# Performance work log

Hardware: AMD Instinct MI355X
Metric: run time of the kernel (lower is better)

## Reference

```python
import jax, jax.numpy as jnp
import numpy as np


def setup_inputs() -> dict:
    key = jax.random.key(0)
    ks = jax.random.split(key, 8)
    B, N = 4, 256
    E, C, H = 64, 128, 256
    return {
        "edge_features": jax.random.normal(ks[0], (B, E, N, N), dtype=jnp.float32),
        "node_features": jax.random.normal(ks[1], (B, C, N), dtype=jnp.float32),
        "W1": jax.random.normal(ks[2], (H, E + 2 * C), dtype=jnp.float32) * 0.05,
        "b1": jax.random.normal(ks[3], (H,), dtype=jnp.float32) * 0.05,
        "W2": jax.random.normal(ks[4], (H, H), dtype=jnp.float32) * 0.05,
        "b2": jax.random.normal(ks[5], (H,), dtype=jnp.float32) * 0.05,
        "W3": jax.random.normal(ks[6], (1, H), dtype=jnp.float32) * 0.05,
        "b3": jax.random.normal(ks[7], (1,), dtype=jnp.float32) * 0.05,
    }


def reference(edge_features, node_features, W1, b1, W2, b2, W3, b3):
    B, C, N = node_features.shape
    # node_addon_row: [B, C, N, N] broadcast along last dim; col along dim 2
    row = jnp.broadcast_to(node_features[:, :, :, None], (B, C, N, N))
    col = jnp.broadcast_to(node_features[:, :, None, :], (B, C, N, N))
    x = jnp.concatenate([edge_features, row, col], axis=1)  # [B, E+2C, N, N]
    # 1x1 conv == channel matmul
    x = jax.nn.relu(jnp.einsum('bcnm,oc->bonm', x, W1) + b1[None, :, None, None])
    x = jax.nn.relu(jnp.einsum('bcnm,oc->bonm', x, W2) + b2[None, :, None, None])
    x = jnp.einsum('bcnm,oc->bonm', x, W3) + b3[None, :, None, None]  # [B,1,N,N]
    return x[:, 0, :, :]
```

## Files before the change

kernel.cpp:

```cpp
#include <hip/hip_runtime.h>
#include <stdint.h>

typedef __bf16 bf16x8 __attribute__((ext_vector_type(8)));
typedef __bf16 bf16x4v __attribute__((ext_vector_type(4)));
typedef float  f32x16 __attribute__((ext_vector_type(16)));
typedef float  f32x4t __attribute__((ext_vector_type(4)));
typedef unsigned int u32x2 __attribute__((ext_vector_type(2)));

#define WS_W1S 0
#define WS_W2S 32768
#define WS_R   163840
#define WS_CT  1212416

__global__ __launch_bounds__(256) void prep_all(
    const float* __restrict__ W1, const float* __restrict__ b1,
    const float* __restrict__ W2, const float* __restrict__ node,
    __bf16* __restrict__ w1s, __bf16* __restrict__ w2s,
    float* __restrict__ Rt, __bf16* __restrict__ Ctb) {
    __shared__ float nds[128 * 4];
    const int blk = blockIdx.x;
    if (blk < 40) {
        int t = blk * 256 + threadIdx.x;
        int chunk = t >> 6, lane = t & 63;
        if (chunk < 128) {
            int wid = chunk >> 5, ks = (chunk >> 1) & 15, mb = chunk & 1;
            int o = wid * 64 + mb * 32 + (lane & 31);
            int k = ks * 16 + (lane >> 5) * 8;
            const float* src = W2 + o * 256 + k;
            __bf16* dst = w2s + chunk * 512 + lane * 8;
#pragma unroll
            for (int j = 0; j < 8; ++j) dst[j] = (__bf16)src[j];
        } else if (chunk < 160) {
            int c1 = chunk - 128;
            int wid = c1 >> 3, ks = (c1 >> 1) & 3, mb = c1 & 1;
            int o = wid * 64 + mb * 32 + (lane & 31);
            int k = ks * 16 + (lane >> 5) * 8;
            const float* src = W1 + o * 320 + k;
            __bf16* dst = w1s + c1 * 512 + lane * 8;
#pragma unroll
            for (int j = 0; j < 8; ++j) dst[j] = (__bf16)src[j];
        }
        return;
    }
    const int rcb = blk - 40;
    const int b = rcb >> 6, j0 = (rcb & 63) << 2;
    const int o = threadIdx.x;
    if (o < 128)
        *(float4*)&nds[o * 4] = *(const float4*)(node + b * 32768 + o * 256 + j0);
    __syncthreads();
    float aR[4] = {0.f, 0.f, 0.f, 0.f};
    float aC[4] = {0.f, 0.f, 0.f, 0.f};
    const float* wr = W1 + o * 320 + 64;
    const float* wc = W1 + o * 320 + 192;
    for (int c4 = 0; c4 < 32; ++c4) {
        float4 wrv = *(const float4*)(wr + c4 * 4);
        float4 wcv = *(const float4*)(wc + c4 * 4);
        const float* wrp = (const float*)&wrv;
        const float* wcp = (const float*)&wcv;
#pragma unroll
        for (int r = 0; r < 4; ++r) {
            f32x4t n4 = *(const f32x4t*)&nds[(c4 * 4 + r) * 4];
#pragma unroll
            for (int q = 0; q < 4; ++q) {
                aR[q] = fmaf(wrp[r], n4[q], aR[q]);
                aC[q] = fmaf(wcp[r], n4[q], aC[q]);
            }
        }
    }
    float bb = b1[o];
#pragma unroll
    for (int j = 0; j < 4; ++j) {
        int idx = ((b * 256 + j0 + j) << 8) + o;
        Rt[idx] = aR[j] + bb;
        Ctb[idx] = (__bf16)aC[j];
    }
}

__device__ __forceinline__ void lds_barrier() {
    __builtin_amdgcn_sched_barrier(0);
    asm volatile("s_waitcnt lgkmcnt(0)" ::: "memory");
    __builtin_amdgcn_s_barrier();
    __builtin_amdgcn_sched_barrier(0);
}

__global__ __launch_bounds__(256, 2) void fused_main(
    const float* __restrict__ edge, const __bf16* __restrict__ w1s,
    const __bf16* __restrict__ w2s, const float* __restrict__ Rt,
    const __bf16* __restrict__ Ctb, const float* __restrict__ b2,
    const float* __restrict__ W3, const float* __restrict__ b3,
    float* __restrict__ out) {
    __shared__ unsigned int lds_e[64 * 34];
    __shared__ unsigned int lds_h1[64 * 140];
    __shared__ float lds_p[8 * 64 * 9];
    __shared__ float lds_c[512];

    const int tid = threadIdx.x;
    const int wid = tid >> 6;
    const int lane = tid & 63;
    const int p31 = lane & 31;
    const int hi = lane >> 5;
    const int obase = wid * 64;

    const int blk = blockIdx.x;
    const int b   = blk >> 7;
    const int m0  = ((blk >> 5) & 3) << 6;
    const int n0  = (blk & 31) << 3;

    lds_c[tid] = b2[tid];
    lds_c[256 + tid] = W3[tid];

    const float4* eg = (const float4*)edge;
    const int a_ = tid & 15;
    const int epb = tid >> 4;
    float4 pf[4];

#define PREFETCH(nn)                                                        \
    {                                                                       \
        _Pragma("unroll")                                                   \
        for (int r = 0; r < 2; ++r) {                                       \
            int ep = r * 16 + epb;                                          \
            int f4 = (b * 64 + ep * 2) * 16384 + (nn) * 64 + (m0 >> 2) + a_;\
            pf[r * 2]     = eg[f4];                                         \
            pf[r * 2 + 1] = eg[f4 + 16384];                                 \
        }                                                                   \
    }

#define LOAD_Q(bf, q)                                                       \
    {                                                                       \
        _Pragma("unroll")                                                   \
        for (int ksl = 0; ksl < 4; ++ksl)                                   \
            _Pragma("unroll")                                               \
            for (int mb = 0; mb < 2; ++mb)                                  \
                A2q[bf][ksl][mb] = *(const bf16x8*)(w2_s +                  \
                    ((((wid << 4) + (q) * 4 + ksl) << 1) + mb) * 512 + (lane << 3)); \
    }

    PREFETCH(n0);

    bf16x4v CvR[8][2];
#pragma unroll
    for (int mb = 0; mb < 2; ++mb)
#pragma unroll
        for (int rg = 0; rg < 4; ++rg)
#pragma unroll
            for (int nb = 0; nb < 2; ++nb)
                CvR[mb * 4 + rg][nb] = *(const bf16x4v*)(Ctb +
                    ((b * 256 + m0 + nb * 32 + p31) << 8) + obase + mb * 32 + 8 * rg + 4 * hi);

    bf16x8 A1[2][4];
#pragma unroll
    for (int mb = 0; mb < 2; ++mb)
#pragma unroll
        for (int ks = 0; ks < 4; ++ks)
            A1[mb][ks] = *(const bf16x8*)(w1s +
                ((((wid << 2) + ks) << 1) + mb) * 512 + (lane << 3));

    f32x16 acc[2][2];
    bf16x8 A2q[2][4][2];
    for (int it = 0; it < 8; ++it) {
        const int n = n0 + it;

        uint64_t w2a = (uint64_t)w2s;
        asm volatile("" : "+s"(w2a));
        const __bf16* w2_s = (const __bf16*)w2a;

#pragma unroll
        for (int r = 0; r < 2; ++r) {
            int ep = r * 16 + epb;
            const float* p0 = (const float*)&pf[r * 2];
            const float* p1 = (const float*)&pf[r * 2 + 1];
#pragma unroll
            for (int i = 0; i < 4; ++i) {
                union { __bf16 h[2]; unsigned int u; } t;
                t.h[0] = (__bf16)p0[i];
                t.h[1] = (__bf16)p1[i];
                lds_e[(a_ * 4 + i) * 34 + ep] = t.u;
            }
        }
        if (it < 7) PREFETCH(n + 1);

        const int nRow = (b * 256 + n) << 8;
        f32x4t Rv[2][4];
#pragma unroll
        for (int mb = 0; mb < 2; ++mb)
#pragma unroll
            for (int rg = 0; rg < 4; ++rg)
                Rv[mb][rg] = *(const f32x4t*)(Rt + nRow + obase + mb * 32 + 8 * rg + 4 * hi);

#pragma unroll
        for (int mb = 0; mb < 2; ++mb)
#pragma unroll
            for (int nb = 0; nb < 2; ++nb)
#pragma unroll
                for (int rg = 0; rg < 4; ++rg)
#pragma unroll
                    for (int rr = 0; rr < 4; ++rr)
                        acc[mb][nb][rg * 4 + rr] = (float)CvR[mb * 4 + rg][nb][rr];

        lds_barrier();

        __builtin_amdgcn_s_setprio(1);
#pragma unroll
        for (int ks = 0; ks < 4; ++ks) {
            bf16x8 B1[2];
#pragma unroll
            for (int nb = 0; nb < 2; ++nb) {
                union { u32x2 d[2]; bf16x8 v; } bb;
                const unsigned int* base = &lds_e[(nb * 32 + p31) * 34 + ks * 8 + hi * 4];
                bb.d[0] = *(const u32x2*)base;
                bb.d[1] = *(const u32x2*)(base + 2);
                B1[nb] = bb.v;
            }
#pragma unroll
            for (int mb = 0; mb < 2; ++mb) {
                acc[mb][0] = __builtin_amdgcn_mfma_f32_32x32x16_bf16(A1[mb][ks], B1[0], acc[mb][0], 0, 0, 0);
                acc[mb][1] = __builtin_amdgcn_mfma_f32_32x32x16_bf16(A1[mb][ks], B1[1], acc[mb][1], 0, 0, 0);
            }
        }
        __builtin_amdgcn_s_setprio(0);

#pragma unroll
        for (int mb = 0; mb < 2; ++mb) {
#pragma unroll
            for (int rg = 0; rg < 4; ++rg) {
                int och = obase + mb * 32 + 8 * rg + 4 * hi;
                f32x4t Rvv = Rv[mb][rg];
#pragma unroll
                for (int nb = 0; nb < 2; ++nb) {
                    int pix = nb * 32 + p31;
                    union { __bf16 h[4]; u32x2 u; } t;
#pragma unroll
                    for (int rr = 0; rr < 4; ++rr) {
                        float v = acc[mb][nb][rg * 4 + rr] + Rvv[rr];
                        t.h[rr] = (__bf16)fmaxf(v, 0.f);
                    }
                    *(u32x2*)&lds_h1[pix * 140 + (och >> 1)] = t.u;
                }
            }
        }
        LOAD_Q(0, 0);

#pragma unroll
        for (int mb = 0; mb < 2; ++mb)
#pragma unroll
            for (int rg = 0; rg < 4; ++rg) {
                f32x4t b2v = *(const f32x4t*)&lds_c[obase + mb * 32 + 8 * rg + 4 * hi];
#pragma unroll
                for (int nb = 0; nb < 2; ++nb)
#pragma unroll
                    for (int rr = 0; rr < 4; ++rr)
                        acc[mb][nb][rg * 4 + rr] = b2v[rr];
            }

        lds_barrier();

        __builtin_amdgcn_s_setprio(1);
#pragma unroll
        for (int q = 0; q < 4; ++q) {
            if (q < 3) LOAD_Q((q + 1) & 1, q + 1);
#pragma unroll
            for (int ksl = 0; ksl < 4; ++ksl) {
                const int ksg = q * 4 + ksl;
                bf16x8 B2[2];
#pragma unroll
                for (int nb = 0; nb < 2; ++nb)
                    B2[nb] = *(const bf16x8*)&lds_h1[(nb * 32 + p31) * 140 + ksg * 8 + hi * 4];
#pragma unroll
                for (int mb = 0; mb < 2; ++mb) {
                    acc[mb][0] = __builtin_amdgcn_mfma_f32_32x32x16_bf16(A2q[q & 1][ksl][mb], B2[0], acc[mb][0], 0, 0, 0);
                    acc[mb][1] = __builtin_amdgcn_mfma_f32_32x32x16_bf16(A2q[q & 1][ksl][mb], B2[1], acc[mb][1], 0, 0, 0);
                }
            }
        }
        __builtin_amdgcn_s_setprio(0);

        float part0 = 0.f, part1 = 0.f;
#pragma unroll
        for (int mb = 0; mb < 2; ++mb) {
#pragma unroll
            for (int rg = 0; rg < 4; ++rg) {
                int och = obase + mb * 32 + 8 * rg + 4 * hi;
                f32x4t w3v = *(const f32x4t*)&lds_c[256 + och];
#pragma unroll
                for (int rr = 0; rr < 4; ++rr) {
                    float h0 = fmaxf(acc[mb][0][rg * 4 + rr], 0.f);
                    float h1v = fmaxf(acc[mb][1][rg * 4 + rr], 0.f);
                    part0 = fmaf(w3v[rr], h0, part0);
                    part1 = fmaf(w3v[rr], h1v, part1);
                }
            }
        }
        lds_p[(it * 64 + 0 * 32 + p31) * 9 + wid * 2 + hi] = part0;
        lds_p[(it * 64 + 1 * 32 + p31) * 9 + wid * 2 + hi] = part1;
    }

    __syncthreads();
    {
        float bb3 = b3[0];
#pragma unroll
        for (int r = 0; r < 2; ++r) {
            int idx = r * 256 + tid;
            int row = idx >> 6;
            int mm  = idx & 63;
            float s = bb3;
#pragma unroll
            for (int k = 0; k < 8; ++k) s += lds_p[(row * 64 + mm) * 9 + k];
            out[((b * 256 + n0 + row) << 8) + m0 + mm] = s;
        }
    }
#undef PREFETCH
#undef LOAD_Q
}

extern "C" void kernel_launch(void* const* d_in, const int* in_sizes, int n_in,
                              void* d_out, int out_size, void* d_ws, size_t ws_size,
                              hipStream_t stream) {
    const float* edge = (const float*)d_in[0];
    const float* node = (const float*)d_in[1];
    const float* W1   = (const float*)d_in[2];
    const float* b1   = (const float*)d_in[3];
    const float* W2   = (const float*)d_in[4];
    const float* b2   = (const float*)d_in[5];
    const float* W3   = (const float*)d_in[6];
    const float* b3   = (const float*)d_in[7];
    char* ws = (char*)d_ws;
    __bf16* w1s = (__bf16*)(ws + WS_W1S);
    __bf16* w2s = (__bf16*)(ws + WS_W2S);
    float*  Rt  = (float*)(ws + WS_R);
    __bf16* Ctb = (__bf16*)(ws + WS_CT);

    prep_all<<<296, 256, 0, stream>>>(W1, b1, W2, node, w1s, w2s, Rt, Ctb);
    fused_main<<<512, 256, 0, stream>>>(edge, w1s, w2s, Rt, Ctb, b2, W3, b3, (float*)d_out);
}
```

Baseline: 151.5 us.

## Use 512-thread blocks processing two rows, stage half of W2 in LDS, atomically reduce output

Doubles the block to eight waves, with two row-groups sharing one set of W1/W2 fragments, and halves the grid. The upper half of the W2 K-dimension is staged once into LDS and read from there, which cuts register pressure and global reloads of W2. The per-tile cross-wave partial-sum buffer and final reduction are replaced by a shuffle and atomicAdd into the output, which prep_all now pre-initialises with b3. The cost is much larger LDS use per block (about 64KB for W2), which may limit occupancy, plus atomic contention on the output.

```diff
diff --git a/kernel.cpp b/kernel.cpp
--- a/kernel.cpp
+++ b/kernel.cpp
@@ -15,10 +15,17 @@
 __global__ __launch_bounds__(256) void prep_all(
     const float* __restrict__ W1, const float* __restrict__ b1,
     const float* __restrict__ W2, const float* __restrict__ node,
-    __bf16* __restrict__ w1s, __bf16* __restrict__ w2s,
-    float* __restrict__ Rt, __bf16* __restrict__ Ctb) {
+    const float* __restrict__ b3, __bf16* __restrict__ w1s,
+    __bf16* __restrict__ w2s, float* __restrict__ Rt,
+    __bf16* __restrict__ Ctb, float* __restrict__ out) {
     __shared__ float nds[128 * 4];
     const int blk = blockIdx.x;
+    if (blk >= 296) {
+        float v = b3[0];
+        float4 f4 = make_float4(v, v, v, v);
+        *(float4*)(out + (blk - 296) * 1024 + threadIdx.x * 4) = f4;
+        return;
+    }
     if (blk < 40) {
         int t = blk * 256 + threadIdx.x;
         int chunk = t >> 6, lane = t & 63;
@@ -83,35 +90,51 @@
     __builtin_amdgcn_sched_barrier(0);
 }
 
-__global__ __launch_bounds__(256, 2) void fused_main(
+__global__ __launch_bounds__(512, 2) void fused_main(
     const float* __restrict__ edge, const __bf16* __restrict__ w1s,
     const __bf16* __restrict__ w2s, const float* __restrict__ Rt,
     const __bf16* __restrict__ Ctb, const float* __restrict__ b2,
     const float* __restrict__ W3, const float* __restrict__ b3,
     float* __restrict__ out) {
-    __shared__ unsigned int lds_e[64 * 34];
-    __shared__ unsigned int lds_h1[64 * 140];
-    __shared__ float lds_p[8 * 64 * 9];
+    __shared__ __bf16 w2lds[32768];
+    __shared__ unsigned int lds_e[128 * 34];
+    __shared__ unsigned int lds_h1[2][64 * 140];
     __shared__ float lds_c[512];
 
     const int tid = threadIdx.x;
-    const int wid = tid >> 6;
+    const int wid8 = tid >> 6;
+    const int og   = wid8 & 3;
+    const int rw   = wid8 >> 2;
     const int lane = tid & 63;
-    const int p31 = lane & 31;
-    const int hi = lane >> 5;
-    const int obase = wid * 64;
+    const int p31  = lane & 31;
+    const int hi   = lane >> 5;
+    const int obase = og << 6;
 
     const int blk = blockIdx.x;
-    const int b   = blk >> 7;
-    const int m0  = ((blk >> 5) & 3) << 6;
-    const int n0  = (blk & 31) << 3;
-
-    lds_c[tid] = b2[tid];
-    lds_c[256 + tid] = W3[tid];
+    const int b   = blk >> 6;
+    const int m0  = ((blk >> 4) & 3) << 6;
+    const int n0  = (blk & 15) << 4;
+
+    lds_c[tid] = (tid < 256) ? b2[tid] : W3[tid - 256];
+
+    {
+        bf16x8 wt[8];
+#pragma unroll
+        for (int i = 0; i < 8; ++i) {
+            int rc = wid8 * 8 + i;
+            int mb = rc & 1, k8 = (rc >> 1) & 7, wg = rc >> 4;
+            int schunk = (((wg << 4) + 8 + k8) << 1) + mb;
+            wt[i] = *(const bf16x8*)(w2s + schunk * 512 + (lane << 3));
+        }
+#pragma unroll
+        for (int i = 0; i < 8; ++i)
+            *(bf16x8*)(w2lds + (wid8 * 8 + i) * 512 + (lane << 3)) = wt[i];
+    }
 
     const float4* eg = (const float4*)edge;
-    const int a_ = tid & 15;
-    const int epb = tid >> 4;
+    const int tid8 = tid & 255;
+    const int a_   = tid8 & 15;
+    const int epb  = tid8 >> 4;
     float4 pf[4];
 
 #define PREFETCH(nn)                                                        \
@@ -132,10 +155,10 @@
             _Pragma("unroll")                                               \
             for (int mb = 0; mb < 2; ++mb)                                  \
                 A2q[bf][ksl][mb] = *(const bf16x8*)(w2_s +                  \
-                    ((((wid << 4) + (q) * 4 + ksl) << 1) + mb) * 512 + (lane << 3)); \
-    }
-
-    PREFETCH(n0);
+                    ((((og << 4) + (q) * 4 + ksl) << 1) + mb) * 512 + (lane << 3)); \
+    }
+
+    PREFETCH(n0 + rw);
 
     bf16x4v CvR[8][2];
 #pragma unroll
@@ -153,16 +176,19 @@
 #pragma unroll
         for (int ks = 0; ks < 4; ++ks)
             A1[mb][ks] = *(const bf16x8*)(w1s +
-                ((((wid << 2) + ks) << 1) + mb) * 512 + (lane << 3));
+                ((((og << 2) + ks) << 1) + mb) * 512 + (lane << 3));
 
     f32x16 acc[2][2];
     bf16x8 A2q[2][4][2];
-    for (int it = 0; it < 8; ++it) {
-        const int n = n0 + it;
+#pragma unroll 1
+    for (int itp = 0; itp < 8; ++itp) {
+        const int n_r = n0 + itp * 2 + rw;
 
         uint64_t w2a = (uint64_t)w2s;
         asm volatile("" : "+s"(w2a));
         const __bf16* w2_s = (const __bf16*)w2a;
+        int koff = 0;
+        asm volatile("" : "+v"(koff));
 
 #pragma unroll
         for (int r = 0; r < 2; ++r) {
@@ -174,12 +200,12 @@
                 union { __bf16 h[2]; unsigned int u; } t;
                 t.h[0] = (__bf16)p0[i];
                 t.h[1] = (__bf16)p1[i];
-                lds_e[(a_ * 4 + i) * 34 + ep] = t.u;
-            }
-        }
-        if (it < 7) PREFETCH(n + 1);
-
-        const int nRow = (b * 256 + n) << 8;
+                lds_e[(rw * 64 + a_ * 4 + i) * 34 + ep] = t.u;
+            }
+        }
+        if (itp < 7) PREFETCH(n0 + (itp + 1) * 2 + rw);
+
+        const int nRow = (b * 256 + n_r) << 8;
         f32x4t Rv[2][4];
 #pragma unroll
         for (int mb = 0; mb < 2; ++mb)
@@ -206,7 +232,7 @@
 #pragma unroll
             for (int nb = 0; nb < 2; ++nb) {
                 union { u32x2 d[2]; bf16x8 v; } bb;
-                const unsigned int* base = &lds_e[(nb * 32 + p31) * 34 + ks * 8 + hi * 4];
+                const unsigned int* base = &lds_e[(rw * 64 + nb * 32 + p31) * 34 + ks * 8 + hi * 4];
                 bb.d[0] = *(const u32x2*)base;
                 bb.d[1] = *(const u32x2*)(base + 2);
                 B1[nb] = bb.v;
@@ -234,7 +260,7 @@
                         float v = acc[mb][nb][rg * 4 + rr] + Rvv[rr];
                         t.h[rr] = (__bf16)fmaxf(v, 0.f);
                     }
-                    *(u32x2*)&lds_h1[pix * 140 + (och >> 1)] = t.u;
+                    *(u32x2*)&lds_h1[rw][pix * 140 + (och >> 1)] = t.u;
                 }
             }
         }
@@ -256,20 +282,38 @@
 
         __builtin_amdgcn_s_setprio(1);
 #pragma unroll
-        for (int q = 0; q < 4; ++q) {
-            if (q < 3) LOAD_Q((q + 1) & 1, q + 1);
+        for (int q = 0; q < 2; ++q) {
+            if (q == 0) LOAD_Q(1, 1);
 #pragma unroll
             for (int ksl = 0; ksl < 4; ++ksl) {
                 const int ksg = q * 4 + ksl;
                 bf16x8 B2[2];
 #pragma unroll
                 for (int nb = 0; nb < 2; ++nb)
-                    B2[nb] = *(const bf16x8*)&lds_h1[(nb * 32 + p31) * 140 + ksg * 8 + hi * 4];
+                    B2[nb] = *(const bf16x8*)&lds_h1[rw][(nb * 32 + p31) * 140 + ksg * 8 + hi * 4];
 #pragma unroll
                 for (int mb = 0; mb < 2; ++mb) {
-                    acc[mb][0] = __builtin_amdgcn_mfma_f32_32x32x16_bf16(A2q[q & 1][ksl][mb], B2[0], acc[mb][0], 0, 0, 0);
-                    acc[mb][1] = __builtin_amdgcn_mfma_f32_32x32x16_bf16(A2q[q & 1][ksl][mb], B2[1], acc[mb][1], 0, 0, 0);
+                    acc[mb][0] = __builtin_amdgcn_mfma_f32_32x32x16_bf16(A2q[q][ksl][mb], B2[0], acc[mb][0], 0, 0, 0);
+                    acc[mb][1] = __builtin_amdgcn_mfma_f32_32x32x16_bf16(A2q[q][ksl][mb], B2[1], acc[mb][1], 0, 0, 0);
                 }
+            }
+        }
+#pragma unroll
+        for (int k8 = 0; k8 < 8; ++k8) {
+            const int ksg = 8 + k8;
+            bf16x8 A2r[2];
+#pragma unroll
+            for (int mb = 0; mb < 2; ++mb)
+                A2r[mb] = *(const bf16x8*)(w2lds +
+                    (((og * 8 + k8) * 2 + mb) * 512 + koff) + (lane << 3));
+            bf16x8 B2[2];
+#pragma unroll
+            for (int nb = 0; nb < 2; ++nb)
+                B2[nb] = *(const bf16x8*)&lds_h1[rw][(nb * 32 + p31) * 140 + ksg * 8 + hi * 4];
+#pragma unroll
+            for (int mb = 0; mb < 2; ++mb) {
+                acc[mb][0] = __builtin_amdgcn_mfma_f32_32x32x16_bf16(A2r[mb], B2[0], acc[mb][0], 0, 0, 0);
+                acc[mb][1] = __builtin_amdgcn_mfma_f32_32x32x16_bf16(A2r[mb], B2[1], acc[mb][1], 0, 0, 0);
             }
         }
         __builtin_amdgcn_s_setprio(0);
@@ -290,22 +334,12 @@
                 }
             }
         }
-        lds_p[(it * 64 + 0 * 32 + p31) * 9 + wid * 2 + hi] = part0;
-        lds_p[(it * 64 + 1 * 32 + p31) * 9 + wid * 2 + hi] = part1;
-    }
-
-    __syncthreads();
-    {
-        float bb3 = b3[0];
-#pragma unroll
-        for (int r = 0; r < 2; ++r) {
-            int idx = r * 256 + tid;
-            int row = idx >> 6;
-            int mm  = idx & 63;
-            float s = bb3;
-#pragma unroll
-            for (int k = 0; k < 8; ++k) s += lds_p[(row * 64 + mm) * 9 + k];
-            out[((b * 256 + n0 + row) << 8) + m0 + mm] = s;
+        part0 += __shfl_xor(part0, 32);
+        part1 += __shfl_xor(part1, 32);
+        {
+            int pix = hi ? (32 + p31) : p31;
+            float v = hi ? part1 : part0;
+            atomicAdd(&out[((b * 256 + n_r) << 8) + m0 + pix], v);
         }
     }
 #undef PREFETCH
@@ -328,7 +362,8 @@
     __bf16* w2s = (__bf16*)(ws + WS_W2S);
     float*  Rt  = (float*)(ws + WS_R);
     __bf16* Ctb = (__bf16*)(ws + WS_CT);
-
-    prep_all<<<296, 256, 0, stream>>>(W1, b1, W2, node, w1s, w2s, Rt, Ctb);
-    fused_main<<<512, 256, 0, stream>>>(edge, w1s, w2s, Rt, Ctb, b2, W3, b3, (float*)d_out);
+    float* outp = (float*)d_out;
+
+    prep_all<<<552, 256, 0, stream>>>(W1, b1, W2, node, b3, w1s, w2s, Rt, Ctb, outp);
+    fused_main<<<256, 512, 0, stream>>>(edge, w1s, w2s, Rt, Ctb, b2, W3, b3, outp);
 }
```

New measurement: 148.6 us. No clear change (-1.9%).
